# Optimization experiments

Measured on AMD Instinct MI355X. Metric: run time of the kernel, lower is better.

## Reference

```python
import jax, jax.numpy as jnp
import numpy as np

N_HEADS = 12

def setup_inputs() -> dict:
    key = jax.random.key(0)
    k1, k2, k3 = jax.random.split(key, 3)
    B, L, D = 2, 2048, 768
    x = jax.random.normal(k1, (B, L, D), dtype=jnp.float32)
    attention_mask = jnp.ones((B, L), dtype=jnp.int32)  # 1 = real token
    w_qkv = jax.random.normal(k2, (D, 3 * D), dtype=jnp.float32) * (1.0 / np.sqrt(D))
    b_qkv = jnp.zeros((3 * D,), dtype=jnp.float32)
    w_out = jax.random.normal(k3, (D, D), dtype=jnp.float32) * (1.0 / np.sqrt(D))
    b_out = jnp.zeros((D,), dtype=jnp.float32)
    return {"x": x, "attention_mask": attention_mask, "w_qkv": w_qkv,
            "b_qkv": b_qkv, "w_out": w_out, "b_out": b_out}

def reference(x, attention_mask, w_qkv, b_qkv, w_out, b_out):
    B, L, D = x.shape
    H = N_HEADS
    dk = D // H
    # fused QKV projection
    qkv = jnp.einsum('bld,de->ble', x, w_qkv) + b_qkv  # (B,L,3D)
    q, k, v = jnp.split(qkv, 3, axis=-1)
    def to_heads(t):
        return t.reshape(B, L, H, dk).transpose(0, 2, 1, 3)  # (B,H,L,dk)
    q, k, v = to_heads(q), to_heads(k), to_heads(v)
    scale = 1.0 / jnp.sqrt(jnp.asarray(dk, dtype=x.dtype))
    scores = jnp.einsum('bhqd,bhkd->bhqk', q, k) * scale  # (B,H,L,L)
    mask = (attention_mask != 0)[:, None, None, :]  # (B,1,1,L), True = keep
    neg = jnp.asarray(jnp.finfo(scores.dtype).min, dtype=scores.dtype)
    scores = jnp.where(mask, scores, neg)
    weights = jax.nn.softmax(scores, axis=-1)
    out = jnp.einsum('bhqk,bhkd->bhqd', weights, v)  # (B,H,L,dk)
    out = out.transpose(0, 2, 1, 3).reshape(B, L, D)
    return jnp.einsum('bld,de->ble', out, w_out) + b_out
```

## Files before the change

### kernel.cpp

```cpp
#include <hip/hip_runtime.h>

typedef __bf16 bf16;
typedef bf16 bf16x4 __attribute__((ext_vector_type(4)));
typedef bf16 bf16x8 __attribute__((ext_vector_type(8)));
typedef float f32x4 __attribute__((ext_vector_type(4)));

#define MFMA16(A, B, C) __builtin_amdgcn_mfma_f32_16x16x32_bf16(A, B, C, 0, 0, 0)
#define NEG_BIG -30000.0f

#define GLOAD_LDS16(gptr, lptr)                                                \
    __builtin_amdgcn_global_load_lds(                                          \
        (__attribute__((address_space(1))) void*)(gptr),                       \
        (__attribute__((address_space(3))) void*)(lptr), 16, 0, 0)

#define SW(r, c8) ((r) * 64 + (((((c8) >> 3) ^ ((r) & 7))) << 3))
#define SW32(r, q) ((r) * 32 + ((((q) ^ ((r) & 3))) << 3))

__global__ void mark_k(float* __restrict__ out, float val, int n) {
    int i = blockIdx.x * 256 + threadIdx.x;
    if (i < n) out[i] = val;
}

__global__ __launch_bounds__(256) void cvt_x_k(const float* __restrict__ src,
                                               bf16* __restrict__ dst, int n) {
    int i = (blockIdx.x * 256 + threadIdx.x) * 8;
    if (i >= n) return;
    float4 a = *(const float4*)&src[i];
    float4 b = *(const float4*)&src[i + 4];
    bf16x8 w;
    w[0] = (bf16)a.x; w[1] = (bf16)a.y; w[2] = (bf16)a.z; w[3] = (bf16)a.w;
    w[4] = (bf16)b.x; w[5] = (bf16)b.y; w[6] = (bf16)b.z; w[7] = (bf16)b.w;
    *(bf16x8*)&dst[i] = w;
}

__global__ __launch_bounds__(256) void transpose_cvt_tiled(
    const float* __restrict__ src, bf16* __restrict__ dst, int R, int C) {
    __shared__ float t[32][33];
    int tid = threadIdx.x, tx = tid & 31, ty = tid >> 5;
    int bx = blockIdx.x * 32, by = blockIdx.y * 32;
#pragma unroll
    for (int i = 0; i < 4; ++i) {
        int row = by + ty + i * 8;
        t[ty + i * 8][tx] = src[(size_t)row * C + bx + tx];
    }
    __syncthreads();
#pragma unroll
    for (int i = 0; i < 4; ++i) {
        int outrow = bx + ty + i * 8;
        dst[(size_t)outrow * R + by + tx] = (bf16)t[tx][ty + i * 8];
    }
}

#define CLD 136

__global__ __launch_bounds__(256) void gemm_qkv_v5(
    const bf16* __restrict__ A, const bf16* __restrict__ B,
    const float* __restrict__ bias, bf16* __restrict__ Qh,
    bf16* __restrict__ Kh, bf16* __restrict__ Vth) {
    __shared__ __align__(16) bf16 SMEM[128 * CLD];
    int tid = threadIdx.x, lane = tid & 63, wave = tid >> 6;
    int quad = lane >> 4, l16 = lane & 15;
    int wr = wave >> 1, wc = wave & 1;
    int m0 = blockIdx.y * 128, n0 = blockIdx.x * 128;
    const int K = 768;
    const f32x4 fz = {0.f, 0.f, 0.f, 0.f};
    f32x4 acc[4][4];
#pragma unroll
    for (int nj = 0; nj < 4; ++nj)
#pragma unroll
        for (int mi = 0; mi < 4; ++mi) acc[nj][mi] = fz;
    const bf16* Ablk = A + (size_t)m0 * K;
    const bf16* Bblk = B + (size_t)n0 * K;
    int srow = lane >> 2, c = lane & 3;

#pragma unroll
    for (int i = 0; i < 2; ++i) {
        int r0 = i * 64 + wave * 16;
        int row = r0 + srow;
        int sc = (c ^ (row & 3)) << 3;
        GLOAD_LDS16(&Ablk[(size_t)row * K + sc], &SMEM[r0 * 32]);
        GLOAD_LDS16(&Bblk[(size_t)row * K + sc], &SMEM[4096 + r0 * 32]);
    }

    int p = 0;
    for (int k0 = 0; k0 < K; k0 += 32) {
        __syncthreads();
        if (k0 + 32 < K) {
            int kn = k0 + 32;
#pragma unroll
            for (int i = 0; i < 2; ++i) {
                int r0 = i * 64 + wave * 16;
                int row = r0 + srow;
                int sc = (c ^ (row & 3)) << 3;
                GLOAD_LDS16(&Ablk[(size_t)row * K + kn + sc],
                            &SMEM[(1 - p) * 8192 + r0 * 32]);
                GLOAD_LDS16(&Bblk[(size_t)row * K + kn + sc],
                            &SMEM[4096 + (1 - p) * 8192 + r0 * 32]);
            }
        }
        const bf16* Asp = &SMEM[p * 8192];
        const bf16* Bsp = &SMEM[4096 + p * 8192];
        bf16x8 af[4], bfv[4];
#pragma unroll
        for (int t = 0; t < 4; ++t) {
            af[t]  = *(const bf16x8*)&Asp[SW32(wr * 64 + t * 16 + l16, quad)];
            bfv[t] = *(const bf16x8*)&Bsp[SW32(wc * 64 + t * 16 + l16, quad)];
        }
#pragma unroll
        for (int nj = 0; nj < 4; ++nj)
#pragma unroll
            for (int mi = 0; mi < 4; ++mi)
                acc[nj][mi] = MFMA16(bfv[nj], af[mi], acc[nj][mi]);
        p ^= 1;
    }

    int which = n0 / 768;
    int h0 = (n0 % 768) >> 6;
    int b = m0 >> 11, l0 = m0 & 2047;
    __syncthreads();

    if (which == 2) {
#pragma unroll
        for (int nj = 0; nj < 4; ++nj) {
            int cl0 = wc * 64 + nj * 16 + quad * 4;
            float4 bv4 = *(const float4*)&bias[n0 + cl0];
            float bv[4] = {bv4.x, bv4.y, bv4.z, bv4.w};
#pragma unroll
            for (int mi = 0; mi < 4; ++mi) {
                int xrl = wr * 64 + mi * 16 + l16;
#pragma unroll
                for (int r = 0; r < 4; ++r)
                    SMEM[(cl0 + r) * CLD + xrl] = (bf16)(acc[nj][mi][r] + bv[r]);
            }
        }
    } else {
        float s = (which == 0) ? 0.18033688f : 1.0f;
#pragma unroll
        for (int nj = 0; nj < 4; ++nj) {
            int cl0 = wc * 64 + nj * 16 + quad * 4;
            float4 bv4 = *(const float4*)&bias[n0 + cl0];
            float bv[4] = {bv4.x, bv4.y, bv4.z, bv4.w};
#pragma unroll
            for (int mi = 0; mi < 4; ++mi) {
                int xrl = wr * 64 + mi * 16 + l16;
                bf16x4 v;
#pragma unroll
                for (int r = 0; r < 4; ++r) v[r] = (bf16)((acc[nj][mi][r] + bv[r]) * s);
                *(bf16x4*)&SMEM[xrl * CLD + cl0] = v;
            }
        }
    }
    __syncthreads();

    if (which == 2) {
#pragma unroll
        for (int i = 0; i < 8; ++i) {
            int idx = i * 256 + tid;
            int cl = idx >> 4, ch = idx & 15;
            int d = cl & 63, h = h0 + (cl >> 6);
            bf16x8 v = *(const bf16x8*)&SMEM[cl * CLD + ch * 8];
            *(bf16x8*)&Vth[((size_t)(b * 12 + h) * 64 + d) * 2048 + l0 + ch * 8] = v;
        }
    } else {
        bf16* dst = (which == 0) ? Qh : Kh;
#pragma unroll
        for (int i = 0; i < 8; ++i) {
            int idx = i * 256 + tid;
            int rr = idx >> 4, ch = idx & 15;
            int h = h0 + (ch >> 3), d0 = (ch & 7) * 8;
            bf16x8 v = *(const bf16x8*)&SMEM[rr * CLD + ch * 8];
            *(bf16x8*)&dst[((size_t)(b * 12 + h) * 2048 + l0 + rr) * 64 + d0] = v;
        }
    }
}

__global__ __launch_bounds__(128) void gemm_out_v4(
    const bf16* __restrict__ A, const bf16* __restrict__ B,
    const float* __restrict__ bias, float* __restrict__ C) {
    __shared__ __align__(16) bf16 As[2][128 * 32];
    __shared__ __align__(16) bf16 Bs[2][64 * 32];
    int tid = threadIdx.x, lane = tid & 63, wave = tid >> 6;
    int quad = lane >> 4, l16 = lane & 15;
    int m0 = blockIdx.y * 128, n0 = blockIdx.x * 64;
    const int K = 768, N = 768;
    const f32x4 fz = {0.f, 0.f, 0.f, 0.f};
    f32x4 acc[4][4];
#pragma unroll
    for (int mi = 0; mi < 4; ++mi)
#pragma unroll
        for (int nj = 0; nj < 4; ++nj) acc[mi][nj] = fz;
    const bf16* Ablk = A + (size_t)m0 * K;
    const bf16* Bblk = B + (size_t)n0 * K;
    int srow = lane >> 2, c = lane & 3;

#pragma unroll
    for (int i = 0; i < 4; ++i) {
        int r0 = i * 32 + wave * 16;
        int row = r0 + srow;
        int sc = (c ^ (row & 3)) << 3;
        GLOAD_LDS16(&Ablk[(size_t)row * K + sc], &As[0][r0 * 32]);
    }
#pragma unroll
    for (int i = 0; i < 2; ++i) {
        int r0 = i * 32 + wave * 16;
        int row = r0 + srow;
        int sc = (c ^ (row & 3)) << 3;
        GLOAD_LDS16(&Bblk[(size_t)row * K + sc], &Bs[0][r0 * 32]);
    }

    int p = 0;
    for (int k0 = 0; k0 < K; k0 += 32) {
        __syncthreads();
        if (k0 + 32 < K) {
            int kn = k0 + 32;
#pragma unroll
            for (int i = 0; i < 4; ++i) {
                int r0 = i * 32 + wave * 16;
                int row = r0 + srow;
                int sc = (c ^ (row & 3)) << 3;
                GLOAD_LDS16(&Ablk[(size_t)row * K + kn + sc], &As[1 - p][r0 * 32]);
            }
#pragma unroll
            for (int i = 0; i < 2; ++i) {
                int r0 = i * 32 + wave * 16;
                int row = r0 + srow;
                int sc = (c ^ (row & 3)) << 3;
                GLOAD_LDS16(&Bblk[(size_t)row * K + kn + sc], &Bs[1 - p][r0 * 32]);
            }
        }
        bf16x8 af[4], bfv[4];
#pragma unroll
        for (int t = 0; t < 4; ++t) {
            af[t]  = *(const bf16x8*)&As[p][SW32(wave * 64 + t * 16 + l16, quad)];
            bfv[t] = *(const bf16x8*)&Bs[p][SW32(t * 16 + l16, quad)];
        }
#pragma unroll
        for (int mi = 0; mi < 4; ++mi)
#pragma unroll
            for (int nj = 0; nj < 4; ++nj)
                acc[mi][nj] = MFMA16(af[mi], bfv[nj], acc[mi][nj]);
        p ^= 1;
    }

#pragma unroll
    for (int nj = 0; nj < 4; ++nj) {
        int col = n0 + nj * 16 + l16;
        float bv = bias[col];
#pragma unroll
        for (int mi = 0; mi < 4; ++mi)
#pragma unroll
            for (int r = 0; r < 4; ++r) {
                int row = m0 + wave * 64 + mi * 16 + quad * 4 + r;
                C[(size_t)row * N + col] = acc[mi][nj][r] + bv;
            }
    }
}

__global__ __launch_bounds__(256) void flash_attn(
    const bf16* __restrict__ Q, const bf16* __restrict__ K,
    const bf16* __restrict__ V, const int* __restrict__ mask,
    bf16* __restrict__ po0, bf16* __restrict__ po1, float* __restrict__ lbuf) {
    __shared__ __align__(16) bf16 Ks[2][64 * 64];
    __shared__ __align__(16) bf16 Vs[2][64 * 64];
    __shared__ float maskS[1024];
    __shared__ int cleanF;

    int tid = threadIdx.x, lane = tid & 63, wave = tid >> 6;
    int quad = lane >> 4, l16 = lane & 15;

    int n = blockIdx.x;
    int xcd = n & 7, idx = n >> 3;
    int g = xcd * 6 + (idx >> 4);
    int m = idx & 15;
    int bh = g % 24;
    int split = g / 24;
    int b = bh / 12;
    int s0 = split * 1024;
    int q0 = m * 128 + wave * 32;

    bf16x8 aq[2][2];
#pragma unroll
    for (int qt = 0; qt < 2; ++qt) {
        const bf16* Qp = Q + ((size_t)bh * 2048 + q0 + qt * 16 + l16) * 64;
        aq[qt][0] = *(const bf16x8*)(Qp + quad * 8);
        aq[qt][1] = *(const bf16x8*)(Qp + 32 + quad * 8);
    }

    if (tid == 0) cleanF = 1;
    __syncthreads();
    const int* mrow = mask + b * 2048 + s0;
    int myclean = 1;
#pragma unroll
    for (int i = 0; i < 4; ++i) {
        int idx2 = i * 256 + tid;
        int mv = mrow[idx2];
        maskS[idx2] = mv ? 0.0f : NEG_BIG;
        myclean &= (mv != 0);
    }
    if (!myclean) cleanF = 0;

    const f32x4 fz = {0.f, 0.f, 0.f, 0.f};
    f32x4 o[2][4];
    float l_i[2] = {0.f, 0.f};
#pragma unroll
    for (int qt = 0; qt < 2; ++qt)
#pragma unroll
        for (int dt = 0; dt < 4; ++dt) o[qt][dt] = fz;

    int srow = tid >> 3;
    int sc8  = (tid & 7) * 8;
    const bf16* Kbase = K + ((size_t)bh * 2048 + s0) * 64;
    const bf16* Vbase = V + (size_t)bh * 64 * 2048 + s0;

#pragma unroll
    for (int i = 0; i < 2; ++i) {
        int row = srow + i * 32;
        *(bf16x8*)&Ks[0][SW(row, sc8)] =
            *(const bf16x8*)&Kbase[(size_t)row * 64 + sc8];
        *(bf16x8*)&Vs[0][SW(row, sc8)] =
            *(const bf16x8*)&Vbase[(size_t)row * 2048 + sc8];
    }
    __syncthreads();
    int clean = cleanF;

    int p = 0;
    for (int kb = 0; kb < 1024; kb += 64) {
        bf16x8 kreg[2], vreg[2];
        const int pref = (kb + 64 < 1024);
        if (pref) {
            int nb = kb + 64;
#pragma unroll
            for (int i = 0; i < 2; ++i) {
                int row = srow + i * 32;
                kreg[i] = *(const bf16x8*)&Kbase[(size_t)(nb + row) * 64 + sc8];
                vreg[i] = *(const bf16x8*)&Vbase[(size_t)row * 2048 + nb + sc8];
            }
        }

        f32x4 s[2][4];
#pragma unroll
        for (int ct = 0; ct < 4; ++ct) {
            int krow = ct * 16 + l16;
            bf16x8 kf0 = *(const bf16x8*)&Ks[p][SW(krow, quad * 8)];
            bf16x8 kf1 = *(const bf16x8*)&Ks[p][SW(krow, 32 + quad * 8)];
#pragma unroll
            for (int qt = 0; qt < 2; ++qt) {
                f32x4 t = fz;
                t = MFMA16(kf0, aq[qt][0], t);
                t = MFMA16(kf1, aq[qt][1], t);
                s[qt][ct] = t;
            }
        }

        if (!clean) {
#pragma unroll
            for (int ct = 0; ct < 4; ++ct) {
                float4 mv = *(const float4*)&maskS[kb + ct * 16 + quad * 4];
                float ma[4] = {mv.x, mv.y, mv.z, mv.w};
#pragma unroll
                for (int qt = 0; qt < 2; ++qt)
#pragma unroll
                    for (int r = 0; r < 4; ++r) s[qt][ct][r] += ma[r];
            }
        }

        bf16x8 vf[2][4];
#pragma unroll
        for (int ks = 0; ks < 2; ++ks)
#pragma unroll
            for (int dt = 0; dt < 4; ++dt)
                vf[ks][dt] = *(const bf16x8*)&Vs[p][SW(dt * 16 + l16, ks * 32 + quad * 8)];

#pragma unroll
        for (int qt = 0; qt < 2; ++qt) {
#pragma unroll
            for (int ct = 0; ct < 4; ++ct)
#pragma unroll
                for (int r = 0; r < 4; ++r)
                    s[qt][ct][r] = __builtin_amdgcn_exp2f(s[qt][ct][r]);
            float t0 = (s[qt][0][0] + s[qt][0][1]) + (s[qt][0][2] + s[qt][0][3]);
            float t1 = (s[qt][1][0] + s[qt][1][1]) + (s[qt][1][2] + s[qt][1][3]);
            float t2 = (s[qt][2][0] + s[qt][2][1]) + (s[qt][2][2] + s[qt][2][3]);
            float t3 = (s[qt][3][0] + s[qt][3][1]) + (s[qt][3][2] + s[qt][3][3]);
            l_i[qt] += (t0 + t1) + (t2 + t3);

            unsigned pk0[4], pk1[4];
#pragma unroll
            for (int ct = 0; ct < 4; ++ct) {
                asm("v_cvt_pk_bf16_f32 %0, %1, %2"
                    : "=v"(pk0[ct]) : "v"(s[qt][ct][0]), "v"(s[qt][ct][1]));
                asm("v_cvt_pk_bf16_f32 %0, %1, %2"
                    : "=v"(pk1[ct]) : "v"(s[qt][ct][2]), "v"(s[qt][ct][3]));
            }

#pragma unroll
            for (int ks = 0; ks < 2; ++ks) {
                unsigned a0 = pk0[2 * ks], c0 = pk0[2 * ks + 1];
                unsigned b0 = pk1[2 * ks], d0 = pk1[2 * ks + 1];
                asm("v_permlane32_swap_b32 %0, %1" : "+v"(a0), "+v"(c0));
                asm("v_permlane16_swap_b32 %0, %1" : "+v"(a0), "+v"(c0));
                asm("v_permlane32_swap_b32 %0, %1" : "+v"(b0), "+v"(d0));
                asm("v_permlane16_swap_b32 %0, %1" : "+v"(b0), "+v"(d0));
                union { unsigned u[4]; bf16x8 v; } ap;
                ap.u[0] = a0;
                ap.u[1] = b0;
                ap.u[2] = c0;
                ap.u[3] = d0;
#pragma unroll
                for (int dt = 0; dt < 4; ++dt)
                    o[qt][dt] = MFMA16(ap.v, vf[ks][dt], o[qt][dt]);
            }
        }

        if (pref) {
#pragma unroll
            for (int i = 0; i < 2; ++i) {
                int row = srow + i * 32;
                *(bf16x8*)&Ks[1 - p][SW(row, sc8)] = kreg[i];
                *(bf16x8*)&Vs[1 - p][SW(row, sc8)] = vreg[i];
            }
        }
        __syncthreads();
        p ^= 1;
    }

    int h = bh % 12;
    bf16* obase = split ? po1 : po0;
#pragma unroll
    for (int qt = 0; qt < 2; ++qt) {
        l_i[qt] += __shfl_xor(l_i[qt], 16);
        l_i[qt] += __shfl_xor(l_i[qt], 32);
#pragma unroll
        for (int dt = 0; dt < 4; ++dt)
#pragma unroll
            for (int r = 0; r < 4; ++r) {
                int qrow = q0 + qt * 16 + quad * 4 + r;
                obase[((size_t)b * 2048 + qrow) * 768 + h * 64 + dt * 16 + l16] =
                    (bf16)o[qt][dt][r];
            }
        if (quad == 0) {
            int qrow = q0 + qt * 16 + l16;
            lbuf[((size_t)split * 24 + bh) * 2048 + qrow] = l_i[qt];
        }
    }
}

__global__ __launch_bounds__(256) void merge_k(
    bf16* __restrict__ ctx, const bf16* __restrict__ po1,
    const float* __restrict__ lbuf) {
    int idx = blockIdx.x * 256 + threadIdx.x;
    if (idx >= 4096 * 768 / 8) return;
    size_t i8 = (size_t)idx * 8;
    int row = (int)(i8 / 768);
    int col = (int)(i8 % 768);
    int bh = (row >> 11) * 12 + (col >> 6);
    int qrow = row & 2047;
    float l0 = lbuf[(size_t)bh * 2048 + qrow];
    float l1 = lbuf[(size_t)(24 + bh) * 2048 + qrow];
    float inv = 1.0f / (l0 + l1);
    bf16x8 v0 = *(const bf16x8*)&ctx[i8];
    bf16x8 v1 = *(const bf16x8*)&po1[i8];
    bf16x8 o;
#pragma unroll
    for (int k = 0; k < 8; ++k)
        o[k] = (bf16)(((float)v0[k] + (float)v1[k]) * inv);
    *(bf16x8*)&ctx[i8] = o;
}

extern "C" void kernel_launch(void* const* d_in, const int* in_sizes, int n_in,
                              void* d_out, int out_size, void* d_ws, size_t ws_size,
                              hipStream_t stream) {
    float* out = (float*)d_out;

    const float* x = nullptr; const int* mask = nullptr;
    const float* w_qkv = nullptr; const float* b_qkv = nullptr;
    const float* w_out = nullptr; const float* b_out = nullptr;
    int found = 0;
    for (int i = 0; i < n_in; ++i) {
        switch (in_sizes[i]) {
            case 3145728: x     = (const float*)d_in[i]; found |= 1;  break;
            case 4096:    mask  = (const int*)  d_in[i]; found |= 2;  break;
            case 1769472: w_qkv = (const float*)d_in[i]; found |= 4;  break;
            case 2304:    b_qkv = (const float*)d_in[i]; found |= 8;  break;
            case 589824:  w_out = (const float*)d_in[i]; found |= 16; break;
            case 768:     b_out = (const float*)d_in[i]; found |= 32; break;
        }
    }
    if (found != 63) {
        mark_k<<<(out_size + 255) / 256, 256, 0, stream>>>(
            out, 200.0f + (float)found, out_size);
        return;
    }

    const int M = 4096, D = 768, N3 = 2304;
    const size_t HEADS_ELEMS = (size_t)24 * 2048 * 64;

    bf16* ws    = (bf16*)d_ws;
    bf16* Kh    = ws;
    bf16* Vth   = Kh + HEADS_ELEMS;
    bf16* ctx   = Vth + HEADS_ELEMS;
    bf16* wqkvT = ctx + (size_t)M * D;
    bf16* woutT = wqkvT + (size_t)N3 * D;
    bf16* Qh    = (bf16*)d_out;
    bf16* xb    = (bf16*)d_out + HEADS_ELEMS;
    bf16* po1   = xb;
    float* lbuf = (float*)wqkvT;

    cvt_x_k<<<(M * D / 8 + 255) / 256, 256, 0, stream>>>(x, xb, M * D);
    transpose_cvt_tiled<<<dim3(2304 / 32, 768 / 32), 256, 0, stream>>>(
        w_qkv, wqkvT, 768, 2304);
    transpose_cvt_tiled<<<dim3(768 / 32, 768 / 32), 256, 0, stream>>>(
        w_out, woutT, 768, 768);

    gemm_qkv_v5<<<dim3(N3 / 128, M / 128), 256, 0, stream>>>(
        xb, wqkvT, b_qkv, Qh, Kh, Vth);

    flash_attn<<<dim3(768), 256, 0, stream>>>(
        Qh, Kh, Vth, mask, ctx, po1, lbuf);

    merge_k<<<(4096 * 768 / 8 + 255) / 256, 256, 0, stream>>>(ctx, po1, lbuf);

    gemm_out_v4<<<dim3(D / 64, M / 128), 128, 0, stream>>>(
        ctx, woutT, b_out, out);
}
```

Baseline: 174.3 us.

## Remap GEMM block order, retile output GEMM, unroll double-buffer loops, raise attention priority

The QKV GEMM now uses a 1D grid with an XCD-aware block remap, so neighbouring tiles land on the same chiplet and share L2. The output GEMM is retiled to 64x128 blocks with four waves and 384 blocks to raise occupancy, and it gets the same remap. The double-buffered K loops in the GEMMs and in flash attention are unrolled by two so buffer indices become compile-time constants. Flash attention also raises wave priority around its MFMA/softmax section with s_setprio. Together these aim to improve cache locality and occupancy and to cut index arithmetic, at the cost of larger code and a changed tile shape.

```diff
diff --git a/kernel.cpp b/kernel.cpp
--- a/kernel.cpp
+++ b/kernel.cpp
@@ -53,7 +53,7 @@
 
 #define CLD 136
 
-__global__ __launch_bounds__(256) void gemm_qkv_v5(
+__global__ __launch_bounds__(256) void gemm_qkv_v6(
     const bf16* __restrict__ A, const bf16* __restrict__ B,
     const float* __restrict__ bias, bf16* __restrict__ Qh,
     bf16* __restrict__ Kh, bf16* __restrict__ Vth) {
@@ -61,7 +61,9 @@
     int tid = threadIdx.x, lane = tid & 63, wave = tid >> 6;
     int quad = lane >> 4, l16 = lane & 15;
     int wr = wave >> 1, wc = wave & 1;
-    int m0 = blockIdx.y * 128, n0 = blockIdx.x * 128;
+    int t = ((blockIdx.x & 7) * 72) + (blockIdx.x >> 3);
+    int bx = t % 18, by = t / 18;
+    int m0 = by * 128, n0 = bx * 128;
     const int K = 768;
     const f32x4 fz = {0.f, 0.f, 0.f, 0.f};
     f32x4 acc[4][4];
@@ -73,46 +75,38 @@
     const bf16* Bblk = B + (size_t)n0 * K;
     int srow = lane >> 2, c = lane & 3;
 
-#pragma unroll
-    for (int i = 0; i < 2; ++i) {
-        int r0 = i * 64 + wave * 16;
-        int row = r0 + srow;
-        int sc = (c ^ (row & 3)) << 3;
-        GLOAD_LDS16(&Ablk[(size_t)row * K + sc], &SMEM[r0 * 32]);
-        GLOAD_LDS16(&Bblk[(size_t)row * K + sc], &SMEM[4096 + r0 * 32]);
-    }
-
-    int p = 0;
-    for (int k0 = 0; k0 < K; k0 += 32) {
+    auto stage = [&](int kn, int d) {
+#pragma unroll
+        for (int i = 0; i < 2; ++i) {
+            int r0 = i * 64 + wave * 16;
+            int row = r0 + srow;
+            int sc = (c ^ (row & 3)) << 3;
+            GLOAD_LDS16(&Ablk[(size_t)row * K + kn + sc],
+                        &SMEM[d * 8192 + r0 * 32]);
+            GLOAD_LDS16(&Bblk[(size_t)row * K + kn + sc],
+                        &SMEM[4096 + d * 8192 + r0 * 32]);
+        }
+    };
+    stage(0, 0);
+
+    auto body = [&](int k0, int P) {
         __syncthreads();
-        if (k0 + 32 < K) {
-            int kn = k0 + 32;
-#pragma unroll
-            for (int i = 0; i < 2; ++i) {
-                int r0 = i * 64 + wave * 16;
-                int row = r0 + srow;
-                int sc = (c ^ (row & 3)) << 3;
-                GLOAD_LDS16(&Ablk[(size_t)row * K + kn + sc],
-                            &SMEM[(1 - p) * 8192 + r0 * 32]);
-                GLOAD_LDS16(&Bblk[(size_t)row * K + kn + sc],
-                            &SMEM[4096 + (1 - p) * 8192 + r0 * 32]);
-            }
-        }
-        const bf16* Asp = &SMEM[p * 8192];
-        const bf16* Bsp = &SMEM[4096 + p * 8192];
+        if (k0 + 32 < K) stage(k0 + 32, P ^ 1);
+        const bf16* Asp = &SMEM[P * 8192];
+        const bf16* Bsp = &SMEM[4096 + P * 8192];
         bf16x8 af[4], bfv[4];
 #pragma unroll
-        for (int t = 0; t < 4; ++t) {
-            af[t]  = *(const bf16x8*)&Asp[SW32(wr * 64 + t * 16 + l16, quad)];
-            bfv[t] = *(const bf16x8*)&Bsp[SW32(wc * 64 + t * 16 + l16, quad)];
+        for (int tt = 0; tt < 4; ++tt) {
+            af[tt]  = *(const bf16x8*)&Asp[SW32(wr * 64 + tt * 16 + l16, quad)];
+            bfv[tt] = *(const bf16x8*)&Bsp[SW32(wc * 64 + tt * 16 + l16, quad)];
         }
 #pragma unroll
         for (int nj = 0; nj < 4; ++nj)
 #pragma unroll
             for (int mi = 0; mi < 4; ++mi)
                 acc[nj][mi] = MFMA16(bfv[nj], af[mi], acc[nj][mi]);
-        p ^= 1;
-    }
+    };
+    for (int k0 = 0; k0 < K; k0 += 64) { body(k0, 0); body(k0 + 32, 1); }
 
     int which = n0 / 768;
     int h0 = (n0 % 768) >> 6;
@@ -174,83 +168,72 @@
     }
 }
 
-__global__ __launch_bounds__(128) void gemm_out_v4(
+__global__ __launch_bounds__(256) void gemm_out_v5(
     const bf16* __restrict__ A, const bf16* __restrict__ B,
     const float* __restrict__ bias, float* __restrict__ C) {
-    __shared__ __align__(16) bf16 As[2][128 * 32];
-    __shared__ __align__(16) bf16 Bs[2][64 * 32];
+    __shared__ __align__(16) bf16 As[2][64 * 32];
+    __shared__ __align__(16) bf16 Bs[2][128 * 32];
     int tid = threadIdx.x, lane = tid & 63, wave = tid >> 6;
     int quad = lane >> 4, l16 = lane & 15;
-    int m0 = blockIdx.y * 128, n0 = blockIdx.x * 64;
+    int wr = wave >> 1, wc = wave & 1;
+    int t = ((blockIdx.x & 7) * 48) + (blockIdx.x >> 3);
+    int bx = t % 6, by = t / 6;
+    int m0 = by * 64, n0 = bx * 128;
     const int K = 768, N = 768;
     const f32x4 fz = {0.f, 0.f, 0.f, 0.f};
-    f32x4 acc[4][4];
-#pragma unroll
-    for (int mi = 0; mi < 4; ++mi)
+    f32x4 acc[2][4];
+#pragma unroll
+    for (int mi = 0; mi < 2; ++mi)
 #pragma unroll
         for (int nj = 0; nj < 4; ++nj) acc[mi][nj] = fz;
     const bf16* Ablk = A + (size_t)m0 * K;
     const bf16* Bblk = B + (size_t)n0 * K;
     int srow = lane >> 2, c = lane & 3;
 
-#pragma unroll
-    for (int i = 0; i < 4; ++i) {
-        int r0 = i * 32 + wave * 16;
-        int row = r0 + srow;
-        int sc = (c ^ (row & 3)) << 3;
-        GLOAD_LDS16(&Ablk[(size_t)row * K + sc], &As[0][r0 * 32]);
-    }
-#pragma unroll
-    for (int i = 0; i < 2; ++i) {
-        int r0 = i * 32 + wave * 16;
-        int row = r0 + srow;
-        int sc = (c ^ (row & 3)) << 3;
-        GLOAD_LDS16(&Bblk[(size_t)row * K + sc], &Bs[0][r0 * 32]);
-    }
-
-    int p = 0;
-    for (int k0 = 0; k0 < K; k0 += 32) {
+    auto stage = [&](int kn, int d) {
+        {
+            int r0 = wave * 16;
+            int row = r0 + srow;
+            int sc = (c ^ (row & 3)) << 3;
+            GLOAD_LDS16(&Ablk[(size_t)row * K + kn + sc], &As[d][r0 * 32]);
+        }
+#pragma unroll
+        for (int i = 0; i < 2; ++i) {
+            int r0 = i * 64 + wave * 16;
+            int row = r0 + srow;
+            int sc = (c ^ (row & 3)) << 3;
+            GLOAD_LDS16(&Bblk[(size_t)row * K + kn + sc], &Bs[d][r0 * 32]);
+        }
+    };
+    stage(0, 0);
+
+    auto body = [&](int k0, int P) {
         __syncthreads();
-        if (k0 + 32 < K) {
-            int kn = k0 + 32;
-#pragma unroll
-            for (int i = 0; i < 4; ++i) {
-                int r0 = i * 32 + wave * 16;
-                int row = r0 + srow;
-                int sc = (c ^ (row & 3)) << 3;
-                GLOAD_LDS16(&Ablk[(size_t)row * K + kn + sc], &As[1 - p][r0 * 32]);
-            }
-#pragma unroll
-            for (int i = 0; i < 2; ++i) {
-                int r0 = i * 32 + wave * 16;
-                int row = r0 + srow;
-                int sc = (c ^ (row & 3)) << 3;
-                GLOAD_LDS16(&Bblk[(size_t)row * K + kn + sc], &Bs[1 - p][r0 * 32]);
-            }
-        }
-        bf16x8 af[4], bfv[4];
-#pragma unroll
-        for (int t = 0; t < 4; ++t) {
-            af[t]  = *(const bf16x8*)&As[p][SW32(wave * 64 + t * 16 + l16, quad)];
-            bfv[t] = *(const bf16x8*)&Bs[p][SW32(t * 16 + l16, quad)];
-        }
-#pragma unroll
-        for (int mi = 0; mi < 4; ++mi)
+        if (k0 + 32 < K) stage(k0 + 32, P ^ 1);
+        bf16x8 af[2], bfv[4];
+#pragma unroll
+        for (int tt = 0; tt < 2; ++tt)
+            af[tt] = *(const bf16x8*)&As[P][SW32(wr * 32 + tt * 16 + l16, quad)];
+#pragma unroll
+        for (int tt = 0; tt < 4; ++tt)
+            bfv[tt] = *(const bf16x8*)&Bs[P][SW32(wc * 64 + tt * 16 + l16, quad)];
+#pragma unroll
+        for (int mi = 0; mi < 2; ++mi)
 #pragma unroll
             for (int nj = 0; nj < 4; ++nj)
                 acc[mi][nj] = MFMA16(af[mi], bfv[nj], acc[mi][nj]);
-        p ^= 1;
-    }
+    };
+    for (int k0 = 0; k0 < K; k0 += 64) { body(k0, 0); body(k0 + 32, 1); }
 
 #pragma unroll
     for (int nj = 0; nj < 4; ++nj) {
-        int col = n0 + nj * 16 + l16;
+        int col = n0 + wc * 64 + nj * 16 + l16;
         float bv = bias[col];
 #pragma unroll
-        for (int mi = 0; mi < 4; ++mi)
+        for (int mi = 0; mi < 2; ++mi)
 #pragma unroll
             for (int r = 0; r < 4; ++r) {
-                int row = m0 + wave * 64 + mi * 16 + quad * 4 + r;
+                int row = m0 + wr * 32 + mi * 16 + quad * 4 + r;
                 C[(size_t)row * N + col] = acc[mi][nj][r] + bv;
             }
     }
@@ -323,10 +306,9 @@
     __syncthreads();
     int clean = cleanF;
 
-    int p = 0;
-    for (int kb = 0; kb < 1024; kb += 64) {
+    auto body = [&](int kb, int P) {
         bf16x8 kreg[2], vreg[2];
-        const int pref = (kb + 64 < 1024);
+        const bool pref = (kb + 64 < 1024);
         if (pref) {
             int nb = kb + 64;
 #pragma unroll
@@ -337,18 +319,19 @@
             }
         }
 
+        __builtin_amdgcn_s_setprio(1);
         f32x4 s[2][4];
 #pragma unroll
         for (int ct = 0; ct < 4; ++ct) {
             int krow = ct * 16 + l16;
-            bf16x8 kf0 = *(const bf16x8*)&Ks[p][SW(krow, quad * 8)];
-            bf16x8 kf1 = *(const bf16x8*)&Ks[p][SW(krow, 32 + quad * 8)];
+            bf16x8 kf0 = *(const bf16x8*)&Ks[P][SW(krow, quad * 8)];
+            bf16x8 kf1 = *(const bf16x8*)&Ks[P][SW(krow, 32 + quad * 8)];
 #pragma unroll
             for (int qt = 0; qt < 2; ++qt) {
-                f32x4 t = fz;
-                t = MFMA16(kf0, aq[qt][0], t);
-                t = MFMA16(kf1, aq[qt][1], t);
-                s[qt][ct] = t;
+                f32x4 tt = fz;
+                tt = MFMA16(kf0, aq[qt][0], tt);
+                tt = MFMA16(kf1, aq[qt][1], tt);
+                s[qt][ct] = tt;
             }
         }
 
@@ -369,7 +352,8 @@
         for (int ks = 0; ks < 2; ++ks)
 #pragma unroll
             for (int dt = 0; dt < 4; ++dt)
-                vf[ks][dt] = *(const bf16x8*)&Vs[p][SW(dt * 16 + l16, ks * 32 + quad * 8)];
+                vf[ks][dt] =
+                    *(const bf16x8*)&Vs[P][SW(dt * 16 + l16, ks * 32 + quad * 8)];
 
 #pragma unroll
         for (int qt = 0; qt < 2; ++qt) {
@@ -411,18 +395,20 @@
                     o[qt][dt] = MFMA16(ap.v, vf[ks][dt], o[qt][dt]);
             }
         }
+        __builtin_amdgcn_s_setprio(0);
 
         if (pref) {
 #pragma unroll
             for (int i = 0; i < 2; ++i) {
                 int row = srow + i * 32;
-                *(bf16x8*)&Ks[1 - p][SW(row, sc8)] = kreg[i];
-                *(bf16x8*)&Vs[1 - p][SW(row, sc8)] = vreg[i];
+                *(bf16x8*)&Ks[P ^ 1][SW(row, sc8)] = kreg[i];
+                *(bf16x8*)&Vs[P ^ 1][SW(row, sc8)] = vreg[i];
             }
         }
         __syncthreads();
-        p ^= 1;
-    }
+    };
+
+    for (int kb = 0; kb < 1024; kb += 128) { body(kb, 0); body(kb + 64, 1); }
 
     int h = bh % 12;
     bf16* obase = split ? po1 : po0;
@@ -512,7 +498,7 @@
     transpose_cvt_tiled<<<dim3(768 / 32, 768 / 32), 256, 0, stream>>>(
         w_out, woutT, 768, 768);
 
-    gemm_qkv_v5<<<dim3(N3 / 128, M / 128), 256, 0, stream>>>(
+    gemm_qkv_v6<<<dim3(576), 256, 0, stream>>>(
         xb, wqkvT, b_qkv, Qh, Kh, Vth);
 
     flash_attn<<<dim3(768), 256, 0, stream>>>(
@@ -520,6 +506,6 @@
 
     merge_k<<<(4096 * 768 / 8 + 255) / 256, 256, 0, stream>>>(ctx, po1, lbuf);
 
-    gemm_out_v4<<<dim3(D / 64, M / 128), 128, 0, stream>>>(
+    gemm_out_v5<<<dim3(384), 256, 0, stream>>>(
         ctx, woutT, b_out, out);
 }
```

After: 174.7 us. Within noise of the previous version (+0.2%).
